# Performance work log

Hardware: AMD Instinct MI355X
Metric: run time of the kernel (lower is better)

Reference implementation:

```python
import jax, jax.numpy as jnp
import numpy as np

B, A, D, H, F = 256, 96, 384, 192, 96   # molecules, atoms, feat, hidden, species-MLP out
S = 4                                   # number of species (H, C, N, O)
E = B * A * 32                          # edges (avg degree 32)
CUTOFF = 5.2


def smooth_cutoff(d, cutoff):
    # Smoothstep-style cutoff: 1 at d=0, smoothly -> 0 at d=cutoff (Smoothstep class, reversed edges)
    x = jnp.clip((cutoff - d) / cutoff, 0.0, 1.0)
    return x ** 3 * (x * (6.0 * x - 15.0) + 10.0)


def setup_inputs() -> dict:
    key = jax.random.key(0)
    ks = jax.random.split(key, 9)
    species = jax.random.randint(ks[0], (B, A), 0, S, dtype=jnp.int32)
    in_features = jax.random.normal(ks[1], (B, A, D), dtype=jnp.float32)
    atom_index12 = jax.random.randint(ks[2], (2, E), 0, B * A, dtype=jnp.int32)
    distances = jax.random.uniform(ks[3], (E,), jnp.float32, 0.1, CUTOFF)
    total_charges = jnp.zeros((B,), jnp.float32)
    W1 = jax.random.normal(ks[4], (S, D, H), jnp.float32) / np.float32(np.sqrt(D))
    W2 = jax.random.normal(ks[5], (S, H, F), jnp.float32) / np.float32(np.sqrt(H))
    Wn = jax.random.normal(ks[6], (S, F, F), jnp.float32) / np.float32(np.sqrt(F))
    Wf = jax.random.normal(ks[7], (S, 2 * F, 1), jnp.float32) / np.float32(np.sqrt(2 * F))
    return dict(species=species, in_features=in_features, atom_index12=atom_index12,
                distances=distances, total_charges=total_charges,
                W1=W1, W2=W2, Wn=Wn, Wf=Wf,
                decay_prefactor=jnp.asarray(1.0, jnp.float32),
                decay_factor=jnp.asarray(1.0, jnp.float32))


def reference(species, in_features, atom_index12, distances, total_charges,
              W1, W2, Wn, Wf, decay_prefactor, decay_factor):
    b, a, d = in_features.shape
    n = b * a
    sp = species.reshape(-1)                      # [N]
    x = in_features.reshape(n, d)                 # [N, D]

    # per-species main MLP dispatch: internal[i] = MLP_{sp[i]}(x[i])
    internal = jnp.zeros((n, F), x.dtype)
    for s in range(S):
        mask = (sp == s)[:, None]
        h = jax.nn.gelu(x @ W1[s]) @ W2[s]        # [N, F]
        internal = internal + jnp.where(mask, h, jnp.zeros((), x.dtype))

    # per-species neighbor MLP
    nbr = jnp.zeros((n, F), x.dtype)
    for s in range(S):
        mask = (sp == s)[:, None]
        nbr = nbr + jnp.where(mask, internal @ Wn[s], jnp.zeros((), x.dtype))

    # distance-decayed edge messages: merged[i0] += nbr[i1]*w, merged[i1] += nbr[i0]*w
    decay = (decay_prefactor ** 2) * jnp.exp(-(decay_factor ** 2) * distances) \
            * smooth_cutoff(distances, CUTOFF)    # [E]
    i0, i1 = atom_index12[0], atom_index12[1]
    m_to_i0 = nbr[i1] * decay[:, None]            # [E, F]
    m_to_i1 = nbr[i0] * decay[:, None]
    merged = jax.ops.segment_sum(jnp.concatenate([m_to_i0, m_to_i1], axis=0),
                                 jnp.concatenate([i0, i1], axis=0),
                                 num_segments=n)  # [N, F]

    feats = jnp.concatenate([internal, merged], axis=-1)  # [N, 2F]

    # per-species final head -> precharges
    precharges = jnp.zeros((n,), x.dtype)
    for s in range(S):
        mask = (sp == s)
        precharges = precharges + jnp.where(mask, (feats @ Wf[s])[:, 0], jnp.zeros((), x.dtype))
    precharges = precharges.reshape(b, a)

    # total-charge redistribution (uniform factors, no learned redistribution)
    dummy_mask = species != -1
    factors = 1.0 / dummy_mask.sum(-1, keepdims=True).astype(x.dtype)
    charges = precharges + (total_charges - precharges.sum(-1))[:, None] * factors
    charges = jnp.where(dummy_mask, charges, jnp.zeros((), x.dtype))
    return species, charges, precharges
```

## Files before the change

### kernel.cpp

```cpp
#include <hip/hip_runtime.h>
#include <cstdint>
#include <cstddef>

#define NBm 256
#define NAm 96
#define NDm 384
#define NHm 192
#define NFm 96
#define NSm 4
#define NATOMS (NBm*NAm)
#define NEe (NATOMS*32)
#define NMSG (2*NEe)
#define HBLK2 768
#define MCAP 7168
#define CUTOFF_ 5.2f

typedef __attribute__((ext_vector_type(8))) short short8;
typedef __attribute__((ext_vector_type(4))) float float4v;
typedef __attribute__((ext_vector_type(2))) int int2v;

__device__ __forceinline__ short f2bf(float f){
  union { float f; unsigned u; } v; v.f = f;
  unsigned r = v.u + 0x7FFFu + ((v.u >> 16) & 1u);
  return (short)(r >> 16);
}

__device__ __forceinline__ float gelu_t(float x){
  float u = 0.7978845608028654f * (x + 0.044715f * x*x*x);
  float e = __expf(-2.0f * fabsf(u));
  float t = (1.0f - e) / (1.0f + e);
  t = (u >= 0.f) ? t : -t;
  return 0.5f * x * (1.0f + t);
}

#define W1N (NSm*NDm*NHm)
#define W2N (NSm*NHm*NFm)
#define WNN (NSm*NFm*NFm)
__global__ void k_wprep(const float* __restrict__ W1, const float* __restrict__ W2,
                        const float* __restrict__ Wn,
                        short* __restrict__ W1t, short* __restrict__ W2t,
                        short* __restrict__ Wnt, int* __restrict__ spc,
                        int* __restrict__ gcur){
  int idx = blockIdx.x*256 + threadIdx.x;
  if (blockIdx.x == 0 && threadIdx.x < NSm) spc[threadIdx.x] = 0;
  if (idx < NBm*16) gcur[idx] = 0;
  if (idx < W1N){
    int s = idx / (NDm*NHm); int rem = idx - s*NDm*NHm;
    int k = rem / NHm, c = rem - k*NHm;
    W1t[(s*NHm + c)*NDm + k] = f2bf(W1[idx]);
  } else if (idx < W1N + W2N){
    int j = idx - W1N;
    int s = j / (NHm*NFm); int rem = j - s*NHm*NFm;
    int k = rem / NFm, c = rem - k*NFm;
    W2t[(s*NFm + c)*NHm + k] = f2bf(W2[j]);
  } else if (idx < W1N + W2N + WNN){
    int j = idx - W1N - W2N;
    int s = j / (NFm*NFm); int rem = j - s*NFm*NFm;
    int k = rem / NFm, c = rem - k*NFm;
    Wnt[(s*NFm + c)*NFm + k] = f2bf(Wn[j]);
  }
}

__global__ void k_spcount(const int* __restrict__ sp, int* __restrict__ spc){
  __shared__ int h[NSm];
  int t = threadIdx.x;
  if (t < NSm) h[t] = 0;
  __syncthreads();
  int i = blockIdx.x*256 + t;
  atomicAdd(&h[sp[i]], 1);
  __syncthreads();
  if (t < NSm) atomicAdd(&spc[t], h[t]);
}

__global__ void k_spscan(const int* __restrict__ spc, int* __restrict__ sps, int* __restrict__ spcur){
  if (threadIdx.x==0 && blockIdx.x==0){
    int r=0;
    for (int s=0;s<NSm;s++){ sps[s]=r; spcur[s]=r; r+=spc[s]; }
    sps[NSm]=r;
  }
}

__global__ void k_spscatter(const int* __restrict__ sp, int* __restrict__ spcur,
                            int* __restrict__ order){
  __shared__ int h[NSm], base[NSm];
  int t = threadIdx.x;
  if (t < NSm) h[t]=0;
  __syncthreads();
  int i = blockIdx.x*256 + t;
  int s = sp[i];
  int lr = atomicAdd(&h[s], 1);
  __syncthreads();
  if (t < NSm) base[t] = atomicAdd(&spcur[t], h[t]);
  __syncthreads();
  order[base[s] + lr] = i;
}

__global__ __launch_bounds__(256) void k_mlp(
    const float* __restrict__ X, const int* __restrict__ order,
    const int* __restrict__ sps,
    const short* __restrict__ W1t, const short* __restrict__ W2t,
    const short* __restrict__ Wnt, const float* __restrict__ Wf,
    float* __restrict__ pre, float* __restrict__ nbr_g){
  const int s = blockIdx.y;
  const int s0 = sps[s];
  const int cnt = sps[s+1] - s0;
  const int row0 = blockIdx.x * 64;
  if (row0 >= cnt) return;

  __shared__ short Hs[64][200];
  __shared__ short Is[64][104];
  __shared__ short Ws[19968];
  __shared__ int aids[64];

  const int tid = threadIdx.x;
  if (tid < 64){
    int r = row0 + tid;
    aids[tid] = order[s0 + ((r < cnt) ? r : 0)];
  }
  __syncthreads();

  const int wave = tid >> 6, lane = tid & 63;
  const int lrow = lane & 15, quad = lane >> 4;
  const int arow = wave*16 + lrow;
  const float* xrow = X + (size_t)aids[arow]*NDm + quad*8;

  short8 afs[12];
  #pragma unroll
  for (int kb=0; kb<12; kb++){
    const float* p = xrow + kb*32;
    #pragma unroll
    for (int j=0;j<8;j++) afs[kb][j] = f2bf(p[j]);
  }

  const short* W1s = W1t + (size_t)s*NHm*NDm;
  float4v acc[12];
  #pragma unroll
  for (int i=0;i<12;i++){ acc[i][0]=0.f; acc[i][1]=0.f; acc[i][2]=0.f; acc[i][3]=0.f; }
  for (int kc=0; kc<4; kc++){
    __syncthreads();
    for (int e = tid; e < 192*12; e += 256){
      int c = e / 12, u = e - c*12;
      *(short8*)(&Ws[c*104 + u*8]) = *(const short8*)(W1s + c*NDm + kc*96 + u*8);
    }
    __syncthreads();
    #pragma unroll
    for (int kb3=0; kb3<3; kb3++){
      short8 af = afs[kc*3 + kb3];
      #pragma unroll
      for (int ct=0; ct<12; ct++){
        short8 bfb = *(const short8*)(&Ws[(ct*16 + lrow)*104 + kb3*32 + quad*8]);
        acc[ct] = __builtin_amdgcn_mfma_f32_16x16x32_bf16(af, bfb, acc[ct], 0,0,0);
      }
    }
  }
  #pragma unroll
  for (int ct=0; ct<12; ct++){
    #pragma unroll
    for (int r=0;r<4;r++){
      Hs[wave*16 + quad*4 + r][ct*16 + lrow] = f2bf(gelu_t(acc[ct][r]));
    }
  }

  const short* W2s = W2t + (size_t)s*NFm*NHm;
  float4v acc2[6];
  #pragma unroll
  for (int i=0;i<6;i++){ acc2[i][0]=0.f; acc2[i][1]=0.f; acc2[i][2]=0.f; acc2[i][3]=0.f; }
  __syncthreads();
  for (int e = tid; e < 96*24; e += 256){
    int c = e / 24, u = e - c*24;
    *(short8*)(&Ws[c*200 + u*8]) = *(const short8*)(W2s + c*NHm + u*8);
  }
  __syncthreads();
  for (int kb=0; kb<6; kb++){
    short8 af2 = *(const short8*)(&Hs[wave*16 + lrow][kb*32 + quad*8]);
    #pragma unroll
    for (int ct=0; ct<6; ct++){
      short8 bfb = *(const short8*)(&Ws[(ct*16 + lrow)*200 + kb*32 + quad*8]);
      acc2[ct] = __builtin_amdgcn_mfma_f32_16x16x32_bf16(af2, bfb, acc2[ct], 0,0,0);
    }
  }
  #pragma unroll
  for (int ct=0; ct<6; ct++){
    #pragma unroll
    for (int r=0;r<4;r++){
      Is[wave*16 + quad*4 + r][ct*16 + lrow] = f2bf(acc2[ct][r]);
    }
  }

  {
    float pr[4] = {0.f,0.f,0.f,0.f};
    #pragma unroll
    for (int ct=0; ct<6; ct++){
      float wv = Wf[s*2*NFm + ct*16 + lrow];
      #pragma unroll
      for (int r=0;r<4;r++) pr[r] += acc2[ct][r] * wv;
    }
    #pragma unroll
    for (int m=1; m<16; m<<=1){
      #pragma unroll
      for (int r=0;r<4;r++) pr[r] += __shfl_xor(pr[r], m, 64);
    }
    if (lrow == 0){
      #pragma unroll
      for (int r=0;r<4;r++){
        int row = wave*16 + quad*4 + r;
        if (row0 + row < cnt) pre[aids[row]] = pr[r];
      }
    }
  }

  const short* Wns = Wnt + (size_t)s*NFm*NFm;
  float4v acc3[6];
  #pragma unroll
  for (int i=0;i<6;i++){ acc3[i][0]=0.f; acc3[i][1]=0.f; acc3[i][2]=0.f; acc3[i][3]=0.f; }
  __syncthreads();
  for (int e = tid; e < 96*12; e += 256){
    int c = e / 12, u = e - c*12;
    *(short8*)(&Ws[c*104 + u*8]) = *(const short8*)(Wns + c*NFm + u*8);
  }
  __syncthreads();
  for (int kb=0; kb<3; kb++){
    short8 af3 = *(const short8*)(&Is[wave*16 + lrow][kb*32 + quad*8]);
    #pragma unroll
    for (int ct=0; ct<6; ct++){
      short8 bfb = *(const short8*)(&Ws[(ct*16 + lrow)*104 + kb*32 + quad*8]);
      acc3[ct] = __builtin_amdgcn_mfma_f32_16x16x32_bf16(af3, bfb, acc3[ct], 0,0,0);
    }
  }
  #pragma unroll
  for (int ct=0; ct<6; ct++){
    #pragma unroll
    for (int r=0;r<4;r++){
      int row = wave*16 + quad*4 + r, col = ct*16 + lrow;
      if (row0 + row < cnt) nbr_g[(size_t)aids[row]*NFm + col] = acc3[ct][r];
    }
  }
}

__global__ void k_nd4(const float* __restrict__ nbr, const float* __restrict__ Wf,
                      float* __restrict__ nd4){
  int a = blockIdx.x*4 + (threadIdx.x >> 6);
  int lane = threadIdx.x & 63;
  bool lo = lane < 32;
  const float* np = nbr + (size_t)a*NFm;
  float nv1 = np[lane];
  float nv2 = lo ? np[64+lane] : 0.f;
  const float* w0 = Wf + 0*2*NFm + NFm;
  const float* w1 = Wf + 1*2*NFm + NFm;
  const float* w2 = Wf + 2*2*NFm + NFm;
  const float* w3 = Wf + 3*2*NFm + NFm;
  float n0 = nv1*w0[lane] + (lo ? nv2*w0[64+lane] : 0.f);
  float n1 = nv1*w1[lane] + (lo ? nv2*w1[64+lane] : 0.f);
  float n2 = nv1*w2[lane] + (lo ? nv2*w2[64+lane] : 0.f);
  float n3 = nv1*w3[lane] + (lo ? nv2*w3[64+lane] : 0.f);
  #pragma unroll
  for (int m=1; m<64; m<<=1){
    n0 += __shfl_xor(n0, m, 64);
    n1 += __shfl_xor(n1, m, 64);
    n2 += __shfl_xor(n2, m, 64);
    n3 += __shfl_xor(n3, m, 64);
  }
  if (lane == 0){
    float4v v; v[0]=n0; v[1]=n1; v[2]=n2; v[3]=n3;
    *(float4v*)(nd4 + (size_t)a*4) = v;
  }
}

__global__ __launch_bounds__(1024) void k_scatter(const int* __restrict__ ai,
    const float* __restrict__ dist, const float* __restrict__ pref,
    const float* __restrict__ fac, int* __restrict__ gcur, int2v* __restrict__ Msg){
  __shared__ int cnt[NBm];
  __shared__ int base[NBm];
  int t = threadIdx.x;
  if (t < NBm) cnt[t] = 0;
  __syncthreads();
  int bb = blockIdx.x*2048;
  float p = pref[0], fc = fac[0];
  int mols[2], ranks[2]; int2v msgs[2];
  #pragma unroll
  for (int half=0; half<2; half++){
    int m = bb + half*1024 + t;
    int dest = ai[m];
    int other = ai[(m < NEe) ? m + NEe : m - NEe];
    int e = (m < NEe) ? m : m - NEe;
    float d = dist[e];
    float x = (CUTOFF_ - d) * (1.0f/CUTOFF_);
    x = fminf(fmaxf(x, 0.f), 1.f);
    float sc = x*x*x*(x*(6.f*x - 15.f) + 10.f);
    float w = p*p * expf(-fc*fc*d) * sc;
    int mol = dest / NAm, dl = dest - mol*NAm;
    mols[half] = mol;
    ranks[half] = atomicAdd(&cnt[mol], 1);
    msgs[half][0] = (other << 7) | dl; msgs[half][1] = __float_as_int(w);
  }
  __syncthreads();
  if (t < NBm) base[t] = atomicAdd(&gcur[t*16], cnt[t]);
  __syncthreads();
  #pragma unroll
  for (int half=0; half<2; half++){
    Msg[(size_t)mols[half]*MCAP + base[mols[half]] + ranks[half]] = msgs[half];
  }
}

__global__ __launch_bounds__(1024) void k_accum(const int* __restrict__ gcur,
    const int2v* __restrict__ Msg, const float* __restrict__ nd4,
    const int* __restrict__ sp, const float* __restrict__ pre,
    const float* __restrict__ tc, float* __restrict__ out){
  __shared__ float acc[NAm];
  __shared__ int spl[NAm];
  __shared__ float red[128];
  int mol = blockIdx.x, t = threadIdx.x;
  if (t < NAm){ acc[t] = 0.f; spl[t] = sp[mol*NAm + t]; }
  __syncthreads();
  int len = gcur[mol*16];
  const int2v* seg = Msg + (size_t)mol*MCAP;
  for (int i = t; i < len; i += 1024){
    int2v kw = seg[i];
    int key = kw[0]; float w = __int_as_float(kw[1]);
    int dl = key & 127, other = key >> 7;
    float val = w * nd4[(size_t)other*4 + spl[dl]];
    atomicAdd(&acc[dl], val);
  }
  __syncthreads();
  float pch = 0.f;
  if (t < NAm) pch = pre[mol*NAm + t] + acc[t];
  if (t < 128) red[t] = (t < NAm) ? pch : 0.f;
  __syncthreads();
  for (int o=64; o>0; o>>=1){
    if (t < o) red[t] += red[t + o];
    __syncthreads();
  }
  float sum = red[0];
  if (t < NAm){
    float c = pch + (tc[mol] - sum) * (1.0f/96.0f);
    out[mol*NAm + t] = (float)spl[t];
    out[NATOMS + mol*NAm + t] = c;
    out[2*NATOMS + mol*NAm + t] = pch;
  }
}

extern "C" void kernel_launch(void* const* d_in, const int* in_sizes, int n_in,
                              void* d_out, int out_size, void* d_ws, size_t ws_size,
                              hipStream_t stream) {
  const int*   species = (const int*)  d_in[0];
  const float* X       = (const float*)d_in[1];
  const int*   ai      = (const int*)  d_in[2];
  const float* dist    = (const float*)d_in[3];
  const float* tc      = (const float*)d_in[4];
  const float* W1      = (const float*)d_in[5];
  const float* W2      = (const float*)d_in[6];
  const float* Wn      = (const float*)d_in[7];
  const float* Wf      = (const float*)d_in[8];
  const float* pref    = (const float*)d_in[9];
  const float* fac     = (const float*)d_in[10];
  float* out = (float*)d_out;

  char* w = (char*)d_ws;
  auto alloc = [&](size_t bytes)->char*{
    char* p = w; w += (bytes + 255) & ~(size_t)255; return p;
  };
  int*   spc   = (int*)  alloc(64);
  int*   sps   = (int*)  alloc(64);
  int*   spcur = (int*)  alloc(64);
  int*   gcur  = (int*)  alloc((size_t)NBm*16*4);
  int*   order = (int*)  alloc((size_t)NATOMS*4);
  float* nd4   = (float*)alloc((size_t)NATOMS*4*4);
  float* pre   = (float*)alloc((size_t)NATOMS*4);
  float* nbr   = (float*)alloc((size_t)NATOMS*NFm*4);
  short* W1t   = (short*)alloc((size_t)W1N*2);
  short* W2t   = (short*)alloc((size_t)W2N*2);
  short* Wnt   = (short*)alloc((size_t)WNN*2);
  int2v* Msg   = (int2v*)alloc((size_t)NBm*MCAP*8);

  k_wprep<<<(W1N+W2N+WNN)/256, 256, 0, stream>>>(W1, W2, Wn, W1t, W2t, Wnt, spc, gcur);
  k_spcount<<<NATOMS/256, 256, 0, stream>>>(species, spc);
  k_spscan<<<1, 64, 0, stream>>>(spc, sps, spcur);
  k_spscatter<<<NATOMS/256, 256, 0, stream>>>(species, spcur, order);
  dim3 g(NATOMS/64, NSm);
  k_mlp<<<g, 256, 0, stream>>>(X, order, sps, W1t, W2t, Wnt, Wf, pre, nbr);
  k_nd4<<<NATOMS/4, 256, 0, stream>>>(nbr, Wf, nd4);
  k_scatter<<<HBLK2, 1024, 0, stream>>>(ai, dist, pref, fac, gcur, Msg);
  k_accum<<<NBm, 1024, 0, stream>>>(gcur, Msg, nd4, species, pre, tc, out);
}
```

Before: 184.4 us.

## Shrink MLP tile to 32 rows, split columns across waves, read weights from global

The per-species MLP kernel now handles 32 atom rows per block instead of 64. The four waves are arranged as 2 row groups by 2 column groups, and each wave computes half of the output columns of every layer. Weight staging into shared memory, along with its many __syncthreads, is removed; B fragments are read straight from global memory and rely on L2/L1 caching, and the precharge partials are combined through a small shared buffer. The smaller shared footprint and doubled grid aim for higher occupancy and less synchronisation, at the cost of more global weight traffic and each X row being converted by two waves.

```diff
diff --git a/kernel.cpp b/kernel.cpp
--- a/kernel.cpp
+++ b/kernel.cpp
@@ -104,16 +104,16 @@
   const int s = blockIdx.y;
   const int s0 = sps[s];
   const int cnt = sps[s+1] - s0;
-  const int row0 = blockIdx.x * 64;
+  const int row0 = blockIdx.x * 32;
   if (row0 >= cnt) return;
 
-  __shared__ short Hs[64][200];
-  __shared__ short Is[64][104];
-  __shared__ short Ws[19968];
-  __shared__ int aids[64];
+  __shared__ short Hs[32][200];
+  __shared__ short Is[32][104];
+  __shared__ int aids[32];
+  __shared__ float preP[32][2];
 
   const int tid = threadIdx.x;
-  if (tid < 64){
+  if (tid < 32){
     int r = row0 + tid;
     aids[tid] = order[s0 + ((r < cnt) ? r : 0)];
   }
@@ -121,7 +121,8 @@
 
   const int wave = tid >> 6, lane = tid & 63;
   const int lrow = lane & 15, quad = lane >> 4;
-  const int arow = wave*16 + lrow;
+  const int rg = wave & 1, cg = wave >> 1;
+  const int arow = rg*16 + lrow;
   const float* xrow = X + (size_t)aids[arow]*NDm + quad*8;
 
   short8 afs[12];
@@ -132,66 +133,52 @@
     for (int j=0;j<8;j++) afs[kb][j] = f2bf(p[j]);
   }
 
-  const short* W1s = W1t + (size_t)s*NHm*NDm;
-  float4v acc[12];
-  #pragma unroll
-  for (int i=0;i<12;i++){ acc[i][0]=0.f; acc[i][1]=0.f; acc[i][2]=0.f; acc[i][3]=0.f; }
-  for (int kc=0; kc<4; kc++){
-    __syncthreads();
-    for (int e = tid; e < 192*12; e += 256){
-      int c = e / 12, u = e - c*12;
-      *(short8*)(&Ws[c*104 + u*8]) = *(const short8*)(W1s + c*NDm + kc*96 + u*8);
-    }
-    __syncthreads();
-    #pragma unroll
-    for (int kb3=0; kb3<3; kb3++){
-      short8 af = afs[kc*3 + kb3];
-      #pragma unroll
-      for (int ct=0; ct<12; ct++){
-        short8 bfb = *(const short8*)(&Ws[(ct*16 + lrow)*104 + kb3*32 + quad*8]);
-        acc[ct] = __builtin_amdgcn_mfma_f32_16x16x32_bf16(af, bfb, acc[ct], 0,0,0);
-      }
-    }
-  }
-  #pragma unroll
-  for (int ct=0; ct<12; ct++){
+  const short* W1b = W1t + (size_t)s*NHm*NDm + (size_t)(cg*96 + lrow)*NDm + quad*8;
+  float4v acc[6];
+  #pragma unroll
+  for (int i=0;i<6;i++){ acc[i][0]=0.f; acc[i][1]=0.f; acc[i][2]=0.f; acc[i][3]=0.f; }
+  for (int kb=0; kb<12; kb++){
+    short8 af = afs[kb];
+    #pragma unroll
+    for (int ct=0; ct<6; ct++){
+      short8 bfb = *(const short8*)(W1b + (size_t)(ct*16)*NDm + kb*32);
+      acc[ct] = __builtin_amdgcn_mfma_f32_16x16x32_bf16(af, bfb, acc[ct], 0,0,0);
+    }
+  }
+  #pragma unroll
+  for (int ct=0; ct<6; ct++){
     #pragma unroll
     for (int r=0;r<4;r++){
-      Hs[wave*16 + quad*4 + r][ct*16 + lrow] = f2bf(gelu_t(acc[ct][r]));
-    }
-  }
-
-  const short* W2s = W2t + (size_t)s*NFm*NHm;
-  float4v acc2[6];
-  #pragma unroll
-  for (int i=0;i<6;i++){ acc2[i][0]=0.f; acc2[i][1]=0.f; acc2[i][2]=0.f; acc2[i][3]=0.f; }
-  __syncthreads();
-  for (int e = tid; e < 96*24; e += 256){
-    int c = e / 24, u = e - c*24;
-    *(short8*)(&Ws[c*200 + u*8]) = *(const short8*)(W2s + c*NHm + u*8);
-  }
-  __syncthreads();
+      Hs[rg*16 + quad*4 + r][cg*96 + ct*16 + lrow] = f2bf(gelu_t(acc[ct][r]));
+    }
+  }
+  __syncthreads();
+
+  const short* W2b = W2t + (size_t)s*NFm*NHm + (size_t)(cg*48 + lrow)*NHm + quad*8;
+  float4v acc2[3];
+  #pragma unroll
+  for (int i=0;i<3;i++){ acc2[i][0]=0.f; acc2[i][1]=0.f; acc2[i][2]=0.f; acc2[i][3]=0.f; }
   for (int kb=0; kb<6; kb++){
-    short8 af2 = *(const short8*)(&Hs[wave*16 + lrow][kb*32 + quad*8]);
-    #pragma unroll
-    for (int ct=0; ct<6; ct++){
-      short8 bfb = *(const short8*)(&Ws[(ct*16 + lrow)*200 + kb*32 + quad*8]);
+    short8 af2 = *(const short8*)(&Hs[rg*16 + lrow][kb*32 + quad*8]);
+    #pragma unroll
+    for (int ct=0; ct<3; ct++){
+      short8 bfb = *(const short8*)(W2b + (size_t)(ct*16)*NHm + kb*32);
       acc2[ct] = __builtin_amdgcn_mfma_f32_16x16x32_bf16(af2, bfb, acc2[ct], 0,0,0);
     }
   }
   #pragma unroll
-  for (int ct=0; ct<6; ct++){
+  for (int ct=0; ct<3; ct++){
     #pragma unroll
     for (int r=0;r<4;r++){
-      Is[wave*16 + quad*4 + r][ct*16 + lrow] = f2bf(acc2[ct][r]);
+      Is[rg*16 + quad*4 + r][cg*48 + ct*16 + lrow] = f2bf(acc2[ct][r]);
     }
   }
 
   {
     float pr[4] = {0.f,0.f,0.f,0.f};
     #pragma unroll
-    for (int ct=0; ct<6; ct++){
-      float wv = Wf[s*2*NFm + ct*16 + lrow];
+    for (int ct=0; ct<3; ct++){
+      float wv = Wf[s*2*NFm + cg*48 + ct*16 + lrow];
       #pragma unroll
       for (int r=0;r<4;r++) pr[r] += acc2[ct][r] * wv;
     }
@@ -202,36 +189,31 @@
     }
     if (lrow == 0){
       #pragma unroll
-      for (int r=0;r<4;r++){
-        int row = wave*16 + quad*4 + r;
-        if (row0 + row < cnt) pre[aids[row]] = pr[r];
-      }
-    }
-  }
-
-  const short* Wns = Wnt + (size_t)s*NFm*NFm;
-  float4v acc3[6];
-  #pragma unroll
-  for (int i=0;i<6;i++){ acc3[i][0]=0.f; acc3[i][1]=0.f; acc3[i][2]=0.f; acc3[i][3]=0.f; }
-  __syncthreads();
-  for (int e = tid; e < 96*12; e += 256){
-    int c = e / 12, u = e - c*12;
-    *(short8*)(&Ws[c*104 + u*8]) = *(const short8*)(Wns + c*NFm + u*8);
-  }
-  __syncthreads();
+      for (int r=0;r<4;r++) preP[rg*16 + quad*4 + r][cg] = pr[r];
+    }
+  }
+  __syncthreads();
+  if (tid < 32){
+    if (row0 + tid < cnt) pre[aids[tid]] = preP[tid][0] + preP[tid][1];
+  }
+
+  const short* Wnb = Wnt + (size_t)s*NFm*NFm + (size_t)(cg*48 + lrow)*NFm + quad*8;
+  float4v acc3[3];
+  #pragma unroll
+  for (int i=0;i<3;i++){ acc3[i][0]=0.f; acc3[i][1]=0.f; acc3[i][2]=0.f; acc3[i][3]=0.f; }
   for (int kb=0; kb<3; kb++){
-    short8 af3 = *(const short8*)(&Is[wave*16 + lrow][kb*32 + quad*8]);
-    #pragma unroll
-    for (int ct=0; ct<6; ct++){
-      short8 bfb = *(const short8*)(&Ws[(ct*16 + lrow)*104 + kb*32 + quad*8]);
+    short8 af3 = *(const short8*)(&Is[rg*16 + lrow][kb*32 + quad*8]);
+    #pragma unroll
+    for (int ct=0; ct<3; ct++){
+      short8 bfb = *(const short8*)(Wnb + (size_t)(ct*16)*NFm + kb*32);
       acc3[ct] = __builtin_amdgcn_mfma_f32_16x16x32_bf16(af3, bfb, acc3[ct], 0,0,0);
     }
   }
   #pragma unroll
-  for (int ct=0; ct<6; ct++){
+  for (int ct=0; ct<3; ct++){
     #pragma unroll
     for (int r=0;r<4;r++){
-      int row = wave*16 + quad*4 + r, col = ct*16 + lrow;
+      int row = rg*16 + quad*4 + r, col = cg*48 + ct*16 + lrow;
       if (row0 + row < cnt) nbr_g[(size_t)aids[row]*NFm + col] = acc3[ct][r];
     }
   }
@@ -376,7 +358,7 @@
   k_spcount<<<NATOMS/256, 256, 0, stream>>>(species, spc);
   k_spscan<<<1, 64, 0, stream>>>(spc, sps, spcur);
   k_spscatter<<<NATOMS/256, 256, 0, stream>>>(species, spcur, order);
-  dim3 g(NATOMS/64, NSm);
+  dim3 g(NATOMS/32, NSm);
   k_mlp<<<g, 256, 0, stream>>>(X, order, sps, W1t, W2t, Wnt, Wf, pre, nbr);
   k_nd4<<<NATOMS/4, 256, 0, stream>>>(nbr, Wf, nd4);
   k_scatter<<<HBLK2, 1024, 0, stream>>>(ai, dist, pref, fac, gcur, Msg);
```

Result: slower. 210.1 us (+13.9%).
